# Performance work log

Hardware: AMD Instinct MI355X
Metric: run time of the kernel (lower is better)

Reference implementation:

```python
import jax, jax.numpy as jnp
import numpy as np

B, N, C = 16, 2048, 256  # dim=256, hidden_dim=2*dim -> v,gate each width C
LN_EPS = 1e-5


def setup_inputs() -> dict:
    key = jax.random.key(0)
    ks = jax.random.split(key, 6)
    std = 0.02
    return {
        "x": jax.random.normal(ks[0], (B, N, C), dtype=jnp.float32),
        "H": 64,
        "W": 32,
        "ln_w": jnp.ones((C,), jnp.float32),
        "ln_b": jnp.zeros((C,), jnp.float32),
        "w_hidden": jax.random.normal(ks[1], (C, 2 * C), jnp.float32) * std,
        "b_hidden": jnp.zeros((2 * C,), jnp.float32),
        "w_kv": jax.random.normal(ks[2], (C, C), jnp.float32) * std,  # qkv_bias=False
        "gamma": jnp.ones((2, C), jnp.float32),   # torch.ones(2, dim)
        "beta": jnp.zeros((2, C), jnp.float32),   # torch.zeros(2, dim)
        "w_proj": jax.random.normal(ks[3], (C, C), jnp.float32) * std,
        "b_proj": jnp.zeros((C,), jnp.float32),
    }


def reference(x, H, W, ln_w, ln_b, w_hidden, b_hidden, w_kv, gamma, beta, w_proj, b_proj):
    # H, W are unused by the original forward (pos conv is dead code).
    b, n, c = x.shape
    # LayerNorm
    mu = jnp.mean(x, axis=-1, keepdims=True)
    var = jnp.mean(jnp.square(x - mu), axis=-1, keepdims=True)
    normed = (x - mu) * jax.lax.rsqrt(var + LN_EPS) * ln_w + ln_b
    # to_hidden: Linear + SiLU, then chunk into v, gate (each width c)
    h = jax.nn.silu(normed @ w_hidden + b_hidden)
    v, gate = h[..., :c], h[..., c:]
    # kv projection, then offset-scale into q, k
    Z = normed @ w_kv                                  # (b, n, c)
    QK = Z[..., None, :] * gamma + beta                # (b, n, 2, c)
    q, k = QK[..., 0, :], QK[..., 1, :]
    # relu^2 quadratic attention (no softmax)
    attn = jnp.einsum('bid,bjd->bij', q, k) / n        # (b, n, n)
    A = jnp.square(jax.nn.relu(attn))
    V = jnp.einsum('bij,bjd->bid', A, v)               # (b, n, c)
    # SiLU gating, output projection, residual
    out = (V * gate) @ w_proj + b_proj
    return out + x
```

## Files before the change

kernel.cpp:

```cpp
#include <hip/hip_runtime.h>

#define BN 32768
#define NB 16
#define NN 2048
#define CC 256
#define JT 64
#define NTILES (NN / JT)

using short8  = __attribute__((ext_vector_type(8))) short;
using floatx4 = __attribute__((ext_vector_type(4))) float;

__device__ __forceinline__ unsigned short f2bf(float f) {
  unsigned u = __builtin_bit_cast(unsigned, f);
  u += 0x7fffu + ((u >> 16) & 1u);
  return (unsigned short)(u >> 16);
}
__device__ __forceinline__ float bf2f(unsigned short h) {
  unsigned u = ((unsigned)h) << 16;
  return __builtin_bit_cast(float, u);
}
__device__ __forceinline__ unsigned pk4fp8(float a, float b, float c, float d) {
  unsigned u = __builtin_amdgcn_cvt_pk_fp8_f32(c, d, 0, true);
  return __builtin_amdgcn_cvt_pk_fp8_f32(a, b, (int)u, false);
}
__device__ __forceinline__ long lo64(uint4 v) {
  uint2 t; t.x = v.x; t.y = v.y; return __builtin_bit_cast(long, t);
}
__device__ __forceinline__ long hi64(uint4 v) {
  uint2 t; t.x = v.z; t.y = v.w; return __builtin_bit_cast(long, t);
}
__device__ __forceinline__ void gll16(const void* g, void* l) {
  __builtin_amdgcn_global_load_lds(
      (const __attribute__((address_space(1))) void*)g,
      (__attribute__((address_space(3))) void*)l, 16, 0, 0);
}
__device__ __forceinline__ float silu(float h) {
  return h / (1.0f + __expf(-h));
}

__global__ __launch_bounds__(256) void wconv_kernel(
    const float* __restrict__ wh, const float* __restrict__ wkv,
    const float* __restrict__ wp,
    unsigned short* __restrict__ wTh, unsigned short* __restrict__ wTkv,
    unsigned short* __restrict__ wTp) {
  __shared__ float T[64][65];
  int bid = blockIdx.x;
  const float* src; unsigned short* dst; int N, kt, nt;
  if (bid < 32)      { src = wh;  dst = wTh;  N = 512; kt = bid >> 3;        nt = bid & 7; }
  else if (bid < 48) { src = wkv; dst = wTkv; N = 256; kt = (bid - 32) >> 2; nt = (bid - 32) & 3; }
  else               { src = wp;  dst = wTp;  N = 256; kt = (bid - 48) >> 2; nt = (bid - 48) & 3; }
  int k0 = kt * 64, n0 = nt * 64;
  int t = threadIdx.x;
  int r = t >> 2, c0 = (t & 3) * 16;
#pragma unroll
  for (int e = 0; e < 4; ++e)
    *(float4*)(&T[r][c0 + e * 4]) =
        *(const float4*)(src + (size_t)(k0 + r) * N + n0 + c0 + e * 4);
  __syncthreads();
#pragma unroll
  for (int e = 0; e < 16; ++e)
    dst[(size_t)(n0 + r) * 256 + k0 + c0 + e] = f2bf(T[c0 + e][r]);
}

__global__ __launch_bounds__(256) void producer_kernel(
    const float* __restrict__ x, const float* __restrict__ lw,
    const float* __restrict__ lb,
    const unsigned short* __restrict__ wTh, const float* __restrict__ bh,
    const unsigned short* __restrict__ wTkv,
    const float* __restrict__ gamma, const float* __restrict__ beta,
    unsigned char* __restrict__ vB, unsigned short* __restrict__ gout,
    unsigned char* __restrict__ qout, unsigned char* __restrict__ kout) {
  __shared__ unsigned short Al[64 * 256];
  const int t = threadIdx.x;
  const int mb = blockIdx.x * 64;
  {
    int r = t >> 2, q = t & 3;
    const float4* xp = (const float4*)(x + (size_t)(mb + r) * CC + q * 64);
    float s = 0.0f, s2 = 0.0f;
#pragma unroll
    for (int f = 0; f < 16; ++f) {
      float4 v = xp[f];
      s  += v.x + v.y + v.z + v.w;
      s2 += v.x * v.x + v.y * v.y + v.z * v.z + v.w * v.w;
    }
    s  += __shfl_xor(s, 1);  s  += __shfl_xor(s, 2);
    s2 += __shfl_xor(s2, 1); s2 += __shfl_xor(s2, 2);
    float mu = s * (1.0f / CC);
    float rs = rsqrtf(s2 * (1.0f / CC) - mu * mu + 1e-5f);
    const float4* lwp = (const float4*)(lw + q * 64);
    const float4* lbp = (const float4*)(lb + q * 64);
    asm volatile("" ::: "memory");
#pragma unroll
    for (int f = 0; f < 16; ++f) {
      float4 v = xp[f];
      float4 w = lwp[f], b = lbp[f];
      ushort4 o;
      o.x = f2bf((v.x - mu) * rs * w.x + b.x);
      o.y = f2bf((v.y - mu) * rs * w.y + b.y);
      o.z = f2bf((v.z - mu) * rs * w.z + b.z);
      o.w = f2bf((v.w - mu) * rs * w.w + b.w);
      int c16 = q * 8 + (f >> 1);
      *(ushort4*)((char*)Al + r * 512 + ((c16 ^ (r & 7)) * 16) + (f & 1) * 8) = o;
    }
  }
  __syncthreads();
  const int wave = t >> 6, lane = t & 63;
  const int m = lane & 15, g4 = lane >> 4;
  const int sw = (m >> 1) & 3;
  {
    floatx4 acc[4][4] = {};
#pragma unroll
    for (int ks = 0; ks < 8; ++ks) {
      short8 af[4], bf[4];
#pragma unroll
      for (int i = 0; i < 4; ++i)
        af[i] = *(const short8*)((const char*)Al + (i * 16 + m) * 512 +
                                 (((ks * 4 + g4) ^ (m & 7)) * 16));
#pragma unroll
      for (int j = 0; j < 4; ++j)
        bf[j] = *(const short8*)(wTh + (size_t)(wave * 64 + j * 16 + m) * 256 + ks * 32 + g4 * 8);
#pragma unroll
      for (int i = 0; i < 4; ++i)
#pragma unroll
        for (int j = 0; j < 4; ++j)
          acc[i][j] = __builtin_amdgcn_mfma_f32_16x16x32_bf16(af[i], bf[j], acc[i][j], 0, 0, 0);
    }
    const size_t tb = ((size_t)(mb >> 11) * 32 + ((mb & 2047) >> 6)) * 16384;
    const int jp4 = (g4 & 1) * 4;
    const int g4h = g4 >> 1;
#pragma unroll
    for (int j = 0; j < 4; ++j) {
      int col = wave * 64 + j * 16 + m;
      float bv = bh[col];
      size_t colb = tb + (size_t)col * 64;
#pragma unroll
      for (int i = 0; i < 4; ++i) {
        int g4a = ((i * 2 + g4h) & 3) ^ sw;
        int h8 = ((i >> 1) & 1) * 8;
        float s0 = silu(acc[i][j][0] + bv);
        float s1 = silu(acc[i][j][1] + bv);
        float s2 = silu(acc[i][j][2] + bv);
        float s3 = silu(acc[i][j][3] + bv);
        *(unsigned*)(vB + colb + g4a * 16 + h8 + jp4) = pk4fp8(s0, s1, s2, s3);
      }
    }
  }
  {
    floatx4 acc[4][4] = {};
#pragma unroll
    for (int ks = 0; ks < 8; ++ks) {
      short8 af[4], bf[4];
#pragma unroll
      for (int i = 0; i < 4; ++i)
        af[i] = *(const short8*)((const char*)Al + (i * 16 + m) * 512 +
                                 (((ks * 4 + g4) ^ (m & 7)) * 16));
#pragma unroll
      for (int j = 0; j < 4; ++j)
        bf[j] = *(const short8*)(wTh + (size_t)(256 + wave * 64 + j * 16 + m) * 256 + ks * 32 + g4 * 8);
#pragma unroll
      for (int i = 0; i < 4; ++i)
#pragma unroll
        for (int j = 0; j < 4; ++j)
          acc[i][j] = __builtin_amdgcn_mfma_f32_16x16x32_bf16(af[i], bf[j], acc[i][j], 0, 0, 0);
    }
#pragma unroll
    for (int j = 0; j < 4; ++j) {
      int colg = wave * 64 + j * 16 + m;
      float bv = bh[256 + colg];
#pragma unroll
      for (int i = 0; i < 4; ++i)
#pragma unroll
        for (int r = 0; r < 4; ++r) {
          int row = mb + i * 16 + g4 * 4 + r;
          gout[(size_t)row * CC + colg] = f2bf(silu(acc[i][j][r] + bv));
        }
    }
  }
  {
    floatx4 acc[4][4] = {};
#pragma unroll
    for (int ks = 0; ks < 8; ++ks) {
      short8 af[4], bf[4];
#pragma unroll
      for (int i = 0; i < 4; ++i)
        af[i] = *(const short8*)((const char*)Al + (i * 16 + m) * 512 +
                                 (((ks * 4 + g4) ^ (m & 7)) * 16));
#pragma unroll
      for (int j = 0; j < 4; ++j)
        bf[j] = *(const short8*)(wTkv + (size_t)(wave * 64 + j * 16 + m) * 256 + ks * 32 + g4 * 8);
#pragma unroll
      for (int i = 0; i < 4; ++i)
#pragma unroll
        for (int j = 0; j < 4; ++j)
          acc[i][j] = __builtin_amdgcn_mfma_f32_16x16x32_bf16(bf[j], af[i], acc[i][j], 0, 0, 0);
    }
#pragma unroll
    for (int j = 0; j < 4; ++j) {
      int c4 = wave * 64 + j * 16 + g4 * 4;
      float4 g0 = *(const float4*)(gamma + c4);
      float4 b0 = *(const float4*)(beta + c4);
      float4 g1 = *(const float4*)(gamma + CC + c4);
      float4 b1 = *(const float4*)(beta + CC + c4);
      int ks2 = c4 >> 6;
      int hsub = ((c4 >> 5) & 1) * 8 + (c4 & 7);
      int qsub = ((c4 >> 3) & 3) * 16 + hsub;
      int ksub = ((((c4 >> 3) & 3) ^ sw)) * 16 + hsub;
#pragma unroll
      for (int i = 0; i < 4; ++i) {
        int n = mb + i * 16 + m;
        int bb = n >> 11, jj = n & 2047;
        size_t base = (((size_t)bb * 128 + (jj >> 4)) * 4 + ks2) * 1024 + (size_t)m * 64;
        floatx4 z = acc[i][j];
        *(unsigned*)(qout + base + qsub) = pk4fp8(z[0] * g0.x + b0.x, z[1] * g0.y + b0.y,
                                                  z[2] * g0.z + b0.z, z[3] * g0.w + b0.w);
        *(unsigned*)(kout + base + ksub) = pk4fp8(z[0] * g1.x + b1.x, z[1] * g1.y + b1.y,
                                                  z[2] * g1.z + b1.z, z[3] * g1.w + b1.w);
      }
    }
  }
}

__global__ __launch_bounds__(256, 2) void attn_kernel(
    const unsigned char* __restrict__ qB, const unsigned char* __restrict__ kB,
    const unsigned char* __restrict__ vB, const unsigned short* __restrict__ gg,
    unsigned short* __restrict__ og) {
  __shared__ unsigned char Kl[2][16384];
  __shared__ unsigned char Vl[2][16384];
  const int tid = threadIdx.x;
  const int wave = tid >> 6, lane = tid & 63;
  const int m = lane & 15, g4 = lane >> 4;
  const int id = blockIdx.x;
  const int b = id & 15, bx = id >> 4;
  const int i0 = bx * 64;
  const unsigned char* kimg = kB + (size_t)b * 524288;
  const unsigned char* vimg = vB + (size_t)b * 524288;

  const int iblk = bx * 4 + wave;
  uint4 qf[4];
#pragma unroll
  for (int ks2 = 0; ks2 < 4; ++ks2)
    qf[ks2] = *(const uint4*)(qB + ((size_t)(b * 128 + iblk) * 4 + ks2) * 1024 + m * 64 + g4 * 16);

  floatx4 acc[16] = {};
  const int alo = (m + ((g4 & 1) << 5)) << 2;
  const int ahi = alo + 64;
  const int gsw = (g4 ^ ((m >> 1) & 3)) * 16;

  auto stage = [&](int buf, int t) {
    const unsigned char* kt = kimg + (size_t)t * 16384;
    const unsigned char* vt = vimg + (size_t)t * 16384;
#pragma unroll
    for (int it = 0; it < 4; ++it) {
      int o = (it * 256 + tid) * 16;
      gll16(kt + o, &Kl[buf][o]);
      gll16(vt + o, &Vl[buf][o]);
    }
  };

  stage(0, 0);
  for (int t = 0; t < NTILES; ++t) {
    const int cur = t & 1;
    __syncthreads();
    if (t + 1 < NTILES) stage(cur ^ 1, t + 1);
    floatx4 sacc[4] = {};
#pragma unroll
    for (int ks2 = 0; ks2 < 4; ++ks2) {
#pragma unroll
      for (int jf = 0; jf < 4; ++jf) {
        uint4 kf = *(const uint4*)(&Kl[cur][(jf * 4 + ks2) * 1024 + m * 64 + gsw]);
        sacc[jf] = __builtin_amdgcn_mfma_f32_16x16x32_fp8_fp8(
            lo64(kf), lo64(qf[ks2]), sacc[jf], 0, 0, 0);
        sacc[jf] = __builtin_amdgcn_mfma_f32_16x16x32_fp8_fp8(
            hi64(kf), hi64(qf[ks2]), sacc[jf], 0, 0, 0);
      }
    }
    unsigned pk[4];
#pragma unroll
    for (int jf = 0; jf < 4; ++jf) {
      float p0 = fmaxf(sacc[jf][0], 0.0f) * 0.0625f;
      float p1 = fmaxf(sacc[jf][1], 0.0f) * 0.0625f;
      float p2 = fmaxf(sacc[jf][2], 0.0f) * 0.0625f;
      float p3 = fmaxf(sacc[jf][3], 0.0f) * 0.0625f;
      pk[jf] = pk4fp8(p0 * p0, p1 * p1, p2 * p2, p3 * p3);
    }
    long ap[2];
#pragma unroll
    for (int kk = 0; kk < 2; ++kk) {
      int A0 = __builtin_amdgcn_ds_bpermute(alo, (int)pk[2 * kk]);
      int B0 = __builtin_amdgcn_ds_bpermute(alo, (int)pk[2 * kk + 1]);
      int C0 = __builtin_amdgcn_ds_bpermute(ahi, (int)pk[2 * kk]);
      int D0 = __builtin_amdgcn_ds_bpermute(ahi, (int)pk[2 * kk + 1]);
      unsigned lo = (g4 & 2) ? (unsigned)B0 : (unsigned)A0;
      unsigned hi = (g4 & 2) ? (unsigned)D0 : (unsigned)C0;
      ap[kk] = (long)(((unsigned long long)hi << 32) | lo);
    }
#pragma unroll
    for (int cf = 0; cf < 16; ++cf) {
      uint4 vfr = *(const uint4*)(&Vl[cur][cf * 1024 + m * 64 + gsw]);
      acc[cf] = __builtin_amdgcn_mfma_f32_16x16x32_fp8_fp8(ap[0], lo64(vfr), acc[cf], 0, 0, 0);
      acc[cf] = __builtin_amdgcn_mfma_f32_16x16x32_fp8_fp8(ap[1], hi64(vfr), acc[cf], 0, 0, 0);
    }
  }
  const float sc = 1.0f / 16384.0f;
  const size_t bo = (size_t)b * NN * CC;
#pragma unroll
  for (int cf = 0; cf < 16; ++cf)
#pragma unroll
    for (int r = 0; r < 4; ++r) {
      int row = i0 + wave * 16 + g4 * 4 + r;
      int col = cf * 16 + m;
      size_t off = bo + (size_t)row * CC + col;
      og[off] = f2bf(acc[cf][r] * sc * bf2f(gg[off]));
    }
}

__global__ __launch_bounds__(256) void gemm_proj(
    const unsigned short* __restrict__ A, const unsigned short* __restrict__ BT,
    const float* __restrict__ bias, const float* __restrict__ xres,
    float* __restrict__ out) {
  int wave = threadIdx.x >> 6, lane = threadIdx.x & 63;
  int m = lane & 15, g4 = lane >> 4, kb = g4 * 8;
  int m0 = blockIdx.x * 128 + (wave & 1) * 64;
  int n0 = blockIdx.y * 128 + (wave >> 1) * 64;
  floatx4 acc[4][4] = {};
#pragma unroll
  for (int ks = 0; ks < 8; ++ks) {
    short8 af[4], bf[4];
#pragma unroll
    for (int i = 0; i < 4; ++i)
      af[i] = *(const short8*)(A + (size_t)(m0 + i * 16 + m) * CC + ks * 32 + kb);
#pragma unroll
    for (int j = 0; j < 4; ++j)
      bf[j] = *(const short8*)(BT + (size_t)(n0 + j * 16 + m) * CC + ks * 32 + kb);
#pragma unroll
    for (int i = 0; i < 4; ++i)
#pragma unroll
      for (int j = 0; j < 4; ++j)
        acc[i][j] = __builtin_amdgcn_mfma_f32_16x16x32_bf16(af[i], bf[j], acc[i][j], 0, 0, 0);
  }
#pragma unroll
  for (int j = 0; j < 4; ++j) {
    int col = n0 + j * 16 + m;
    float bv = bias[col];
#pragma unroll
    for (int i = 0; i < 4; ++i)
#pragma unroll
      for (int r = 0; r < 4; ++r) {
        int row = m0 + i * 16 + g4 * 4 + r;
        size_t rr = (size_t)row * CC;
        out[rr + col] = acc[i][j][r] + bv + xres[rr + col];
      }
  }
}

extern "C" void kernel_launch(void* const* d_in, const int* in_sizes, int n_in,
                              void* d_out, int out_size, void* d_ws, size_t ws_size,
                              hipStream_t stream) {
  const float* x        = (const float*)d_in[0];
  const float* ln_w     = (const float*)d_in[3];
  const float* ln_b     = (const float*)d_in[4];
  const float* w_hidden = (const float*)d_in[5];
  const float* b_hidden = (const float*)d_in[6];
  const float* w_kv     = (const float*)d_in[7];
  const float* gamma    = (const float*)d_in[8];
  const float* beta     = (const float*)d_in[9];
  const float* w_proj   = (const float*)d_in[10];
  const float* b_proj   = (const float*)d_in[11];
  float* out = (float*)d_out;
  char* ws = (char*)d_ws;

  const size_t SZ = (size_t)BN * CC * 2;
  const size_t HZ = SZ / 2;
  unsigned short* slot0 = (unsigned short*)(ws);
  unsigned short* gbuf  = (unsigned short*)(ws + SZ);
  unsigned char*  qB    = (unsigned char*)(ws + 2 * SZ);
  unsigned char*  kB    = (unsigned char*)(ws + 2 * SZ + HZ);
  unsigned char*  vB    = (unsigned char*)(ws + 2 * SZ + 2 * HZ);
  unsigned short* wTh   = (unsigned short*)(ws + 2 * SZ + 3 * HZ);
  unsigned short* wTkv  = (unsigned short*)(ws + 2 * SZ + 3 * HZ + 512 * 256 * 2);
  unsigned short* wTp   = (unsigned short*)(ws + 2 * SZ + 3 * HZ + 512 * 256 * 2 + 256 * 256 * 2);

  wconv_kernel<<<64, 256, 0, stream>>>(w_hidden, w_kv, w_proj, wTh, wTkv, wTp);
  producer_kernel<<<BN / 64, 256, 0, stream>>>(
      x, ln_w, ln_b, wTh, b_hidden, wTkv, gamma, beta, vB, gbuf, qB, kB);
  attn_kernel<<<512, 256, 0, stream>>>(qB, kB, vB, gbuf, slot0);
  gemm_proj<<<dim3(BN / 128, 2), 256, 0, stream>>>(slot0, wTp, b_proj, x, out);
}
```

Measured before the change: 146.7 us.

## Split attention waves into 2x2 row/column tiles to reuse fragments

Each wave now covers two 16-row query blocks and half of the 256 output channels, where before it owned one row block across all channels. Each V fragment loaded from LDS now feeds two MFMAs, so LDS reads for V per wave are halved. The cost is that QK^T scores are computed twice, once by each channel-half wave, so score MFMAs per block double. Register use for q fragments also rises.

```diff
diff --git a/kernel.cpp b/kernel.cpp
--- a/kernel.cpp
+++ b/kernel.cpp
@@ -229,19 +229,22 @@
   const int tid = threadIdx.x;
   const int wave = tid >> 6, lane = tid & 63;
   const int m = lane & 15, g4 = lane >> 4;
+  const int ih = wave >> 1, ch = wave & 1;
   const int id = blockIdx.x;
   const int b = id & 15, bx = id >> 4;
   const int i0 = bx * 64;
   const unsigned char* kimg = kB + (size_t)b * 524288;
   const unsigned char* vimg = vB + (size_t)b * 524288;
 
-  const int iblk = bx * 4 + wave;
-  uint4 qf[4];
-#pragma unroll
-  for (int ks2 = 0; ks2 < 4; ++ks2)
-    qf[ks2] = *(const uint4*)(qB + ((size_t)(b * 128 + iblk) * 4 + ks2) * 1024 + m * 64 + g4 * 16);
-
-  floatx4 acc[16] = {};
+  uint4 qf[2][4];
+#pragma unroll
+  for (int ib = 0; ib < 2; ++ib)
+#pragma unroll
+    for (int ks2 = 0; ks2 < 4; ++ks2)
+      qf[ib][ks2] = *(const uint4*)(qB +
+          ((size_t)(b * 128 + bx * 4 + ih * 2 + ib) * 4 + ks2) * 1024 + m * 64 + g4 * 16);
+
+  floatx4 acc[8][2] = {};
   const int alo = (m + ((g4 & 1) << 5)) << 2;
   const int ahi = alo + 64;
   const int gsw = (g4 ^ ((m >> 1) & 3)) * 16;
@@ -262,56 +265,74 @@
     const int cur = t & 1;
     __syncthreads();
     if (t + 1 < NTILES) stage(cur ^ 1, t + 1);
-    floatx4 sacc[4] = {};
-#pragma unroll
-    for (int ks2 = 0; ks2 < 4; ++ks2) {
-#pragma unroll
-      for (int jf = 0; jf < 4; ++jf) {
-        uint4 kf = *(const uint4*)(&Kl[cur][(jf * 4 + ks2) * 1024 + m * 64 + gsw]);
-        sacc[jf] = __builtin_amdgcn_mfma_f32_16x16x32_fp8_fp8(
-            lo64(kf), lo64(qf[ks2]), sacc[jf], 0, 0, 0);
-        sacc[jf] = __builtin_amdgcn_mfma_f32_16x16x32_fp8_fp8(
-            hi64(kf), hi64(qf[ks2]), sacc[jf], 0, 0, 0);
-      }
-    }
-    unsigned pk[4];
-#pragma unroll
-    for (int jf = 0; jf < 4; ++jf) {
-      float p0 = fmaxf(sacc[jf][0], 0.0f) * 0.0625f;
-      float p1 = fmaxf(sacc[jf][1], 0.0f) * 0.0625f;
-      float p2 = fmaxf(sacc[jf][2], 0.0f) * 0.0625f;
-      float p3 = fmaxf(sacc[jf][3], 0.0f) * 0.0625f;
-      pk[jf] = pk4fp8(p0 * p0, p1 * p1, p2 * p2, p3 * p3);
-    }
-    long ap[2];
-#pragma unroll
-    for (int kk = 0; kk < 2; ++kk) {
-      int A0 = __builtin_amdgcn_ds_bpermute(alo, (int)pk[2 * kk]);
-      int B0 = __builtin_amdgcn_ds_bpermute(alo, (int)pk[2 * kk + 1]);
-      int C0 = __builtin_amdgcn_ds_bpermute(ahi, (int)pk[2 * kk]);
-      int D0 = __builtin_amdgcn_ds_bpermute(ahi, (int)pk[2 * kk + 1]);
-      unsigned lo = (g4 & 2) ? (unsigned)B0 : (unsigned)A0;
-      unsigned hi = (g4 & 2) ? (unsigned)D0 : (unsigned)C0;
-      ap[kk] = (long)(((unsigned long long)hi << 32) | lo);
-    }
-#pragma unroll
-    for (int cf = 0; cf < 16; ++cf) {
-      uint4 vfr = *(const uint4*)(&Vl[cur][cf * 1024 + m * 64 + gsw]);
-      acc[cf] = __builtin_amdgcn_mfma_f32_16x16x32_fp8_fp8(ap[0], lo64(vfr), acc[cf], 0, 0, 0);
-      acc[cf] = __builtin_amdgcn_mfma_f32_16x16x32_fp8_fp8(ap[1], hi64(vfr), acc[cf], 0, 0, 0);
+    unsigned pk[2][4];
+#pragma unroll
+    for (int jh2 = 0; jh2 < 2; ++jh2) {
+      floatx4 sacc[2][2] = {};
+#pragma unroll
+      for (int ks2 = 0; ks2 < 4; ++ks2)
+#pragma unroll
+        for (int jf2 = 0; jf2 < 2; ++jf2) {
+          int jf = jh2 * 2 + jf2;
+          uint4 kf = *(const uint4*)(&Kl[cur][(jf * 4 + ks2) * 1024 + m * 64 + gsw]);
+          long klo = lo64(kf), khi = hi64(kf);
+#pragma unroll
+          for (int ib = 0; ib < 2; ++ib) {
+            sacc[jf2][ib] = __builtin_amdgcn_mfma_f32_16x16x32_fp8_fp8(
+                klo, lo64(qf[ib][ks2]), sacc[jf2][ib], 0, 0, 0);
+            sacc[jf2][ib] = __builtin_amdgcn_mfma_f32_16x16x32_fp8_fp8(
+                khi, hi64(qf[ib][ks2]), sacc[jf2][ib], 0, 0, 0);
+          }
+        }
+#pragma unroll
+      for (int jf2 = 0; jf2 < 2; ++jf2)
+#pragma unroll
+        for (int ib = 0; ib < 2; ++ib) {
+          float p0 = fmaxf(sacc[jf2][ib][0], 0.0f) * 0.0625f;
+          float p1 = fmaxf(sacc[jf2][ib][1], 0.0f) * 0.0625f;
+          float p2 = fmaxf(sacc[jf2][ib][2], 0.0f) * 0.0625f;
+          float p3 = fmaxf(sacc[jf2][ib][3], 0.0f) * 0.0625f;
+          pk[ib][jh2 * 2 + jf2] = pk4fp8(p0 * p0, p1 * p1, p2 * p2, p3 * p3);
+        }
+    }
+    long ap[2][2];
+#pragma unroll
+    for (int ib = 0; ib < 2; ++ib)
+#pragma unroll
+      for (int kk = 0; kk < 2; ++kk) {
+        int A0 = __builtin_amdgcn_ds_bpermute(alo, (int)pk[ib][2 * kk]);
+        int B0 = __builtin_amdgcn_ds_bpermute(alo, (int)pk[ib][2 * kk + 1]);
+        int C0 = __builtin_amdgcn_ds_bpermute(ahi, (int)pk[ib][2 * kk]);
+        int D0 = __builtin_amdgcn_ds_bpermute(ahi, (int)pk[ib][2 * kk + 1]);
+        unsigned lo = (g4 & 2) ? (unsigned)B0 : (unsigned)A0;
+        unsigned hi = (g4 & 2) ? (unsigned)D0 : (unsigned)C0;
+        ap[ib][kk] = (long)(((unsigned long long)hi << 32) | lo);
+      }
+#pragma unroll
+    for (int cf = 0; cf < 8; ++cf) {
+      int c = ch * 128 + cf * 16 + m;
+      uint4 vfr = *(const uint4*)(&Vl[cur][c * 64 + gsw]);
+      long vlo = lo64(vfr), vhi = hi64(vfr);
+#pragma unroll
+      for (int ib = 0; ib < 2; ++ib) {
+        acc[cf][ib] = __builtin_amdgcn_mfma_f32_16x16x32_fp8_fp8(ap[ib][0], vlo, acc[cf][ib], 0, 0, 0);
+        acc[cf][ib] = __builtin_amdgcn_mfma_f32_16x16x32_fp8_fp8(ap[ib][1], vhi, acc[cf][ib], 0, 0, 0);
+      }
     }
   }
   const float sc = 1.0f / 16384.0f;
   const size_t bo = (size_t)b * NN * CC;
 #pragma unroll
-  for (int cf = 0; cf < 16; ++cf)
-#pragma unroll
-    for (int r = 0; r < 4; ++r) {
-      int row = i0 + wave * 16 + g4 * 4 + r;
-      int col = cf * 16 + m;
-      size_t off = bo + (size_t)row * CC + col;
-      og[off] = f2bf(acc[cf][r] * sc * bf2f(gg[off]));
-    }
+  for (int cf = 0; cf < 8; ++cf)
+#pragma unroll
+    for (int ib = 0; ib < 2; ++ib)
+#pragma unroll
+      for (int r = 0; r < 4; ++r) {
+        int row = i0 + ih * 32 + ib * 16 + g4 * 4 + r;
+        int col = ch * 128 + cf * 16 + m;
+        size_t off = bo + (size_t)row * CC + col;
+        og[off] = f2bf(acc[cf][ib][r] * sc * bf2f(gg[off]));
+      }
 }
 
 __global__ __launch_bounds__(256) void gemm_proj(
```

Measured after the change: 168.0 us. +14.5%, slower.
